# Performance work log

Hardware: AMD Instinct MI355X
Metric: run time of the kernel (lower is better)

## Reference

```python
import jax, jax.numpy as jnp
import numpy as np

H = 256
V = 64
B = 2048
T = 512


def setup_inputs() -> dict:
    key = jax.random.key(0)
    k1, k2, k3 = jax.random.split(key, 3)
    sequential_features = jax.random.normal(k1, (B, T, V), dtype=jnp.float32)
    # kaiming-uniform-like init scale for theta [H, H+V] and theta_dot [1, H]
    bound_t = float(np.sqrt(6.0 / (H + V)))
    theta = jax.random.uniform(k2, (H, H + V), minval=-bound_t, maxval=bound_t, dtype=jnp.float32)
    bound_d = float(np.sqrt(6.0 / H))
    theta_dot = jax.random.uniform(k3, (1, H), minval=-bound_d, maxval=bound_d, dtype=jnp.float32)
    bias = jnp.zeros((1,), dtype=jnp.float32)
    return {"sequential_features": sequential_features, "theta": theta, "bias": bias, "theta_dot": theta_dot}


def reference(sequential_features, theta, bias, theta_dot):
    # sequential_features: [B, T, V]; theta: [H, H+V]; bias: [1]; theta_dot: [1, H]
    Bn = sequential_features.shape[0]
    Hn = theta.shape[0]

    def step(state, token):
        # state: [B, H], token: [B, V]
        st = jnp.concatenate([state, token], axis=1)          # [B, H+V]
        z = st @ theta.T + bias                                # [B, H]
        mean = jnp.mean(z, axis=1, keepdims=True)
        std = jnp.std(z, axis=1, keepdims=True, ddof=1)        # torch.std uses Bessel correction
        z = (z - mean) / std
        return jax.nn.relu(z), None

    xs = jnp.swapaxes(sequential_features, 0, 1)               # [T, B, V]
    init = jnp.zeros((Bn, Hn), dtype=sequential_features.dtype)
    state, _ = jax.lax.scan(step, init, xs)
    logits = jnp.sum(state * theta_dot, axis=1)                # [B]
    return jax.nn.sigmoid(logits)
```

## Files before the change

kernel.cpp:

```cpp
#include <hip/hip_runtime.h>


#define TT 512
#define VV 64
#define HH 256
#define STRD 264

typedef short bf16x8 __attribute__((ext_vector_type(8)));
typedef float f32x4  __attribute__((ext_vector_type(4)));

__device__ __forceinline__ unsigned short f2bf(float f) {
    unsigned int u = __float_as_uint(f);
    return (unsigned short)((u + 0x8000u) >> 16);
}

__device__ __forceinline__ float bf2f(unsigned short u) {
    return __uint_as_float(((unsigned int)u) << 16);
}

__device__ __forceinline__ bf16x8 pack8(float4 a, float4 b) {
    bf16x8 v;
    v[0] = (short)f2bf(a.x); v[1] = (short)f2bf(a.y);
    v[2] = (short)f2bf(a.z); v[3] = (short)f2bf(a.w);
    v[4] = (short)f2bf(b.x); v[5] = (short)f2bf(b.y);
    v[6] = (short)f2bf(b.z); v[7] = (short)f2bf(b.w);
    return v;
}

template <int CTRL>
__device__ __forceinline__ float dppadd(float x) {
    int y = __builtin_amdgcn_update_dpp(0, __float_as_int(x), CTRL, 0xF, 0xF, false);
    return x + __int_as_float(y);
}

template <int CTRL>
__device__ __forceinline__ float dppbcast(float x) {
    int y = __builtin_amdgcn_update_dpp(0, __float_as_int(x), CTRL, 0xF, 0xF, true);
    return __int_as_float(y);
}

__device__ __forceinline__ void barrier_lgkm() {
    asm volatile("s_waitcnt lgkmcnt(0)\n\ts_barrier" ::: "memory");
}

extern "C" __global__ void __launch_bounds__(256, 1)
rnn_scan_kernel(const float* __restrict__ seq,
                const float* __restrict__ theta,
                const float* __restrict__ theta_dot,
                float* __restrict__ out)
{
    __shared__ unsigned short stbuf[2][16][STRD];
    __shared__ __align__(16) float2 partials[64];

    const int tid = threadIdx.x;
    const int w   = tid >> 6;
    const int l   = tid & 63;
    const int q   = l >> 4;
    const int loc = l & 15;
    const int r0  = blockIdx.x << 4;

    bf16x8 bfrag[10][4];
#pragma unroll
    for (int s = 0; s < 4; ++s) {
        const float* trow = theta + (size_t)(w * 64 + s * 16 + loc) * 320;
#pragma unroll
        for (int ks = 0; ks < 10; ++ks) {
            float4 f0 = *(const float4*)(trow + ks * 32 + q * 8);
            float4 f1 = *(const float4*)(trow + ks * 32 + q * 8 + 4);
            bfrag[ks][s] = pack8(f0, f1);
        }
    }

    {
        const int m = tid >> 4, c = (tid & 15) * 16;
        uint4 z = make_uint4(0u, 0u, 0u, 0u);
        *(uint4*)(&stbuf[0][m][c])     = z;
        *(uint4*)(&stbuf[0][m][c + 8]) = z;
    }

    const float* srow = seq + (size_t)(r0 + loc) * (TT * VV);
    float4 tk0 = *(const float4*)(srow + q * 8);
    float4 tk1 = *(const float4*)(srow + q * 8 + 4);
    float4 tk2 = *(const float4*)(srow + 32 + q * 8);
    float4 tk3 = *(const float4*)(srow + 32 + q * 8 + 4);

    __syncthreads();

#pragma unroll 1
    for (int t = 0; t < TT; ++t) {
        unsigned short* stc = &stbuf[t & 1][0][0];
        unsigned short* stn = &stbuf[(t + 1) & 1][0][0];

        bf16x8 a8 = pack8(tk0, tk1);
        bf16x8 a9 = pack8(tk2, tk3);

        if (t + 1 < TT) {
            const float* p = srow + (size_t)(t + 1) * VV;
            tk0 = *(const float4*)(p + q * 8);
            tk1 = *(const float4*)(p + q * 8 + 4);
            tk2 = *(const float4*)(p + 32 + q * 8);
            tk3 = *(const float4*)(p + 32 + q * 8 + 4);
        }

        f32x4 acc[4];
#pragma unroll
        for (int s = 0; s < 4; ++s) { acc[s][0] = 0.f; acc[s][1] = 0.f; acc[s][2] = 0.f; acc[s][3] = 0.f; }

        const unsigned short* arow = stc + loc * STRD;
#pragma unroll
        for (int ks = 0; ks < 8; ++ks) {
            bf16x8 av = *(const bf16x8*)(arow + ks * 32 + q * 8);
#pragma unroll
            for (int s = 0; s < 4; ++s)
                acc[s] = __builtin_amdgcn_mfma_f32_16x16x32_bf16(av, bfrag[ks][s], acc[s], 0, 0, 0);
        }
#pragma unroll
        for (int s = 0; s < 4; ++s)
            acc[s] = __builtin_amdgcn_mfma_f32_16x16x32_bf16(a8, bfrag[8][s], acc[s], 0, 0, 0);
#pragma unroll
        for (int s = 0; s < 4; ++s)
            acc[s] = __builtin_amdgcn_mfma_f32_16x16x32_bf16(a9, bfrag[9][s], acc[s], 0, 0, 0);

        float sum[4], ssq[4];
#pragma unroll
        for (int r = 0; r < 4; ++r) {
            sum[r] = acc[0][r] + acc[1][r] + acc[2][r] + acc[3][r];
            ssq[r] = acc[0][r] * acc[0][r] + acc[1][r] * acc[1][r]
                   + acc[2][r] * acc[2][r] + acc[3][r] * acc[3][r];
        }
#pragma unroll
        for (int r = 0; r < 4; ++r) {
            sum[r] = dppadd<0xB1>(sum[r]);  ssq[r] = dppadd<0xB1>(ssq[r]);
            sum[r] = dppadd<0x4E>(sum[r]);  ssq[r] = dppadd<0x4E>(ssq[r]);
            sum[r] = dppadd<0x124>(sum[r]); ssq[r] = dppadd<0x124>(ssq[r]);
            sum[r] = dppadd<0x128>(sum[r]); ssq[r] = dppadd<0x128>(ssq[r]);
        }
        if (loc < 4)
            partials[((q * 4 + loc) << 2) | w] = make_float2(sum[loc], ssq[loc]);

        barrier_lgkm();

        const int myrow = (q << 2) | (loc & 3);
        float4 pA = *(const float4*)(&partials[myrow << 2]);
        float4 pB = *(const float4*)(&partials[(myrow << 2) | 2]);
        float sumT = (pA.x + pA.z) + (pB.x + pB.z);
        float ssqT = (pA.y + pA.w) + (pB.y + pB.w);
        float mean = sumT * (1.0f / 256.0f);
        float var  = (ssqT - sumT * mean) * (1.0f / 255.0f);
        float rstd = rsqrtf(var);
        float nb   = -mean * rstd;

        float rs[4], nbv[4];
        rs[0] = dppbcast<0x00>(rstd); nbv[0] = dppbcast<0x00>(nb);
        rs[1] = dppbcast<0x55>(rstd); nbv[1] = dppbcast<0x55>(nb);
        rs[2] = dppbcast<0xAA>(rstd); nbv[2] = dppbcast<0xAA>(nb);
        rs[3] = dppbcast<0xFF>(rstd); nbv[3] = dppbcast<0xFF>(nb);

#pragma unroll
        for (int s = 0; s < 4; ++s) {
#pragma unroll
            for (int r = 0; r < 4; ++r) {
                float v = fmaf(acc[s][r], rs[r], nbv[r]);
                v = fmaxf(v, 0.0f);
                stn[(q * 4 + r) * STRD + (w * 64 + s * 16 + loc)] = f2bf(v);
            }
        }
        barrier_lgkm();
    }

    {
        const int m = tid >> 4, c0 = (tid & 15) << 4;
        const unsigned short* sr = &stbuf[0][m][c0];
        float dot = 0.0f;
#pragma unroll
        for (int j = 0; j < 16; ++j)
            dot += bf2f(sr[j]) * theta_dot[c0 + j];
        dot += __shfl_xor(dot, 1, 64);
        dot += __shfl_xor(dot, 2, 64);
        dot += __shfl_xor(dot, 4, 64);
        dot += __shfl_xor(dot, 8, 64);
        if ((tid & 15) == 0)
            out[r0 + m] = 1.0f / (1.0f + expf(-dot));
    }
}

extern "C" void kernel_launch(void* const* d_in, const int* in_sizes, int n_in,
                              void* d_out, int out_size, void* d_ws, size_t ws_size,
                              hipStream_t stream) {
    const float* seq   = (const float*)d_in[0];
    const float* theta = (const float*)d_in[1];
    const float* tdot  = (const float*)d_in[3];
    float* out = (float*)d_out;

    rnn_scan_kernel<<<dim3(128), dim3(256), 0, stream>>>(seq, theta, tdot, out);
}
```

Baseline: 850.7 us.

## Halve rows per block, defer rstd scaling, and precompute token projection off critical path

Each block now handles 8 batch rows instead of 16 and the grid doubles to 256 blocks, padding the MFMA M-dimension with duplicated rows so more CUs run the serial scan. The normalization is split: the state written each step is only mean-centred and ReLU'd, and the per-row rstd is applied to the next step's recurrent matmul result (and to the final dot product), which takes rsqrt and its broadcast off the store path. The token-projection MFMAs for the next step are issued between the partial-sum barrier and the state store to overlap with the reduction. The risks are wasted MFMA work on the padded rows, a bf16 state stored before scaling with a different dynamic range, and higher register pressure under launch_bounds(256,2).

```diff
diff --git a/kernel.cpp b/kernel.cpp
--- a/kernel.cpp
+++ b/kernel.cpp
@@ -3,7 +3,6 @@
 
 #define TT 512
 #define VV 64
-#define HH 256
 #define STRD 264
 
 typedef short bf16x8 __attribute__((ext_vector_type(8)));
@@ -43,7 +42,7 @@
     asm volatile("s_waitcnt lgkmcnt(0)\n\ts_barrier" ::: "memory");
 }
 
-extern "C" __global__ void __launch_bounds__(256, 1)
+extern "C" __global__ void __launch_bounds__(256, 2)
 rnn_scan_kernel(const float* __restrict__ seq,
                 const float* __restrict__ theta,
                 const float* __restrict__ theta_dot,
@@ -51,13 +50,14 @@
 {
     __shared__ unsigned short stbuf[2][16][STRD];
     __shared__ __align__(16) float2 partials[64];
+    __shared__ float rstd_lds[16];
 
     const int tid = threadIdx.x;
     const int w   = tid >> 6;
     const int l   = tid & 63;
     const int q   = l >> 4;
     const int loc = l & 15;
-    const int r0  = blockIdx.x << 4;
+    const int r0  = blockIdx.x << 3;
 
     bf16x8 bfrag[10][4];
 #pragma unroll
@@ -76,14 +76,38 @@
         uint4 z = make_uint4(0u, 0u, 0u, 0u);
         *(uint4*)(&stbuf[0][m][c])     = z;
         *(uint4*)(&stbuf[0][m][c + 8]) = z;
-    }
-
-    const float* srow = seq + (size_t)(r0 + loc) * (TT * VV);
+        *(uint4*)(&stbuf[1][m][c])     = z;
+        *(uint4*)(&stbuf[1][m][c + 8]) = z;
+    }
+
+    const float* srow = seq + (size_t)(r0 + (loc & 7)) * (TT * VV);
     float4 tk0 = *(const float4*)(srow + q * 8);
     float4 tk1 = *(const float4*)(srow + q * 8 + 4);
     float4 tk2 = *(const float4*)(srow + 32 + q * 8);
     float4 tk3 = *(const float4*)(srow + 32 + q * 8 + 4);
 
+    f32x4 acc_t[4];
+    {
+        bf16x8 a8 = pack8(tk0, tk1);
+        bf16x8 a9 = pack8(tk2, tk3);
+        f32x4 zc; zc[0] = 0.f; zc[1] = 0.f; zc[2] = 0.f; zc[3] = 0.f;
+#pragma unroll
+        for (int s = 0; s < 4; ++s) {
+            acc_t[s] = __builtin_amdgcn_mfma_f32_16x16x32_bf16(a8, bfrag[8][s], zc, 0, 0, 0);
+            acc_t[s] = __builtin_amdgcn_mfma_f32_16x16x32_bf16(a9, bfrag[9][s], acc_t[s], 0, 0, 0);
+        }
+    }
+    {
+        const float* p = srow + VV;
+        tk0 = *(const float4*)(p + q * 8);
+        tk1 = *(const float4*)(p + q * 8 + 4);
+        tk2 = *(const float4*)(p + 32 + q * 8);
+        tk3 = *(const float4*)(p + 32 + q * 8 + 4);
+    }
+
+    float rs[4];
+    rs[0] = 1.0f; rs[1] = 1.0f; rs[2] = 1.0f; rs[3] = 1.0f;
+
     __syncthreads();
 
 #pragma unroll 1
@@ -91,17 +115,6 @@
         unsigned short* stc = &stbuf[t & 1][0][0];
         unsigned short* stn = &stbuf[(t + 1) & 1][0][0];
 
-        bf16x8 a8 = pack8(tk0, tk1);
-        bf16x8 a9 = pack8(tk2, tk3);
-
-        if (t + 1 < TT) {
-            const float* p = srow + (size_t)(t + 1) * VV;
-            tk0 = *(const float4*)(p + q * 8);
-            tk1 = *(const float4*)(p + q * 8 + 4);
-            tk2 = *(const float4*)(p + 32 + q * 8);
-            tk3 = *(const float4*)(p + 32 + q * 8 + 4);
-        }
-
         f32x4 acc[4];
 #pragma unroll
         for (int s = 0; s < 4; ++s) { acc[s][0] = 0.f; acc[s][1] = 0.f; acc[s][2] = 0.f; acc[s][3] = 0.f; }
@@ -114,12 +127,12 @@
             for (int s = 0; s < 4; ++s)
                 acc[s] = __builtin_amdgcn_mfma_f32_16x16x32_bf16(av, bfrag[ks][s], acc[s], 0, 0, 0);
         }
+
 #pragma unroll
         for (int s = 0; s < 4; ++s)
-            acc[s] = __builtin_amdgcn_mfma_f32_16x16x32_bf16(a8, bfrag[8][s], acc[s], 0, 0, 0);
-#pragma unroll
-        for (int s = 0; s < 4; ++s)
-            acc[s] = __builtin_amdgcn_mfma_f32_16x16x32_bf16(a9, bfrag[9][s], acc[s], 0, 0, 0);
+#pragma unroll
+            for (int r = 0; r < 4; ++r)
+                acc[s][r] = fmaf(acc[s][r], rs[r], acc_t[s][r]);
 
         float sum[4], ssq[4];
 #pragma unroll
@@ -143,30 +156,61 @@
         const int myrow = (q << 2) | (loc & 3);
         float4 pA = *(const float4*)(&partials[myrow << 2]);
         float4 pB = *(const float4*)(&partials[(myrow << 2) | 2]);
+
+        if (t + 1 < TT) {
+            bf16x8 a8 = pack8(tk0, tk1);
+            bf16x8 a9 = pack8(tk2, tk3);
+            f32x4 zc; zc[0] = 0.f; zc[1] = 0.f; zc[2] = 0.f; zc[3] = 0.f;
+#pragma unroll
+            for (int s = 0; s < 4; ++s) {
+                acc_t[s] = __builtin_amdgcn_mfma_f32_16x16x32_bf16(a8, bfrag[8][s], zc, 0, 0, 0);
+                acc_t[s] = __builtin_amdgcn_mfma_f32_16x16x32_bf16(a9, bfrag[9][s], acc_t[s], 0, 0, 0);
+            }
+            if (t + 2 < TT) {
+                const float* p = srow + (size_t)(t + 2) * VV;
+                tk0 = *(const float4*)(p + q * 8);
+                tk1 = *(const float4*)(p + q * 8 + 4);
+                tk2 = *(const float4*)(p + 32 + q * 8);
+                tk3 = *(const float4*)(p + 32 + q * 8 + 4);
+            }
+        }
+
         float sumT = (pA.x + pA.z) + (pB.x + pB.z);
         float ssqT = (pA.y + pA.w) + (pB.y + pB.w);
         float mean = sumT * (1.0f / 256.0f);
+        float nm   = -mean;
+        float mb[4];
+        mb[0] = dppbcast<0x00>(nm);
+        mb[1] = dppbcast<0x55>(nm);
+        mb[2] = dppbcast<0xAA>(nm);
+        mb[3] = dppbcast<0xFF>(nm);
+
+        if (q < 2) {
+#pragma unroll
+            for (int s = 0; s < 4; ++s)
+#pragma unroll
+                for (int r = 0; r < 4; ++r) {
+                    float v = fmaxf(acc[s][r] + mb[r], 0.0f);
+                    stn[(q * 4 + r) * STRD + (w * 64 + s * 16 + loc)] = f2bf(v);
+                }
+        }
+
         float var  = (ssqT - sumT * mean) * (1.0f / 255.0f);
         float rstd = rsqrtf(var);
-        float nb   = -mean * rstd;
-
-        float rs[4], nbv[4];
-        rs[0] = dppbcast<0x00>(rstd); nbv[0] = dppbcast<0x00>(nb);
-        rs[1] = dppbcast<0x55>(rstd); nbv[1] = dppbcast<0x55>(nb);
-        rs[2] = dppbcast<0xAA>(rstd); nbv[2] = dppbcast<0xAA>(nb);
-        rs[3] = dppbcast<0xFF>(rstd); nbv[3] = dppbcast<0xFF>(nb);
-
-#pragma unroll
-        for (int s = 0; s < 4; ++s) {
-#pragma unroll
-            for (int r = 0; r < 4; ++r) {
-                float v = fmaf(acc[s][r], rs[r], nbv[r]);
-                v = fmaxf(v, 0.0f);
-                stn[(q * 4 + r) * STRD + (w * 64 + s * 16 + loc)] = f2bf(v);
-            }
-        }
+        rs[0] = dppbcast<0x00>(rstd);
+        rs[1] = dppbcast<0x55>(rstd);
+        rs[2] = dppbcast<0xAA>(rstd);
+        rs[3] = dppbcast<0xFF>(rstd);
+
         barrier_lgkm();
     }
+
+    if (w == 0 && loc == 0) {
+#pragma unroll
+        for (int r = 0; r < 4; ++r)
+            rstd_lds[q * 4 + r] = rs[r];
+    }
+    __syncthreads();
 
     {
         const int m = tid >> 4, c0 = (tid & 15) << 4;
@@ -179,8 +223,8 @@
         dot += __shfl_xor(dot, 2, 64);
         dot += __shfl_xor(dot, 4, 64);
         dot += __shfl_xor(dot, 8, 64);
-        if ((tid & 15) == 0)
-            out[r0 + m] = 1.0f / (1.0f + expf(-dot));
+        if ((tid & 15) == 0 && m < 8)
+            out[r0 + m] = 1.0f / (1.0f + expf(-rstd_lds[m] * dot));
     }
 }
 
@@ -192,5 +236,5 @@
     const float* tdot  = (const float*)d_in[3];
     float* out = (float*)d_out;
 
-    rnn_scan_kernel<<<dim3(128), dim3(256), 0, stream>>>(seq, theta, tdot, out);
-}
+    rnn_scan_kernel<<<dim3(256), dim3(256), 0, stream>>>(seq, theta, tdot, out);
+}
```

After: 880.0 us. 3.4% more time.

## Defer layernorm into next step's A-fragment load, removing one barrier per step

Applied to the files above, without the earlier changes.

Each step now stores the raw pre-normalization MFMA outputs to LDS, packed as bf16 with a permuted hidden-column layout. The next step computes mean and rstd from double-buffered partials and applies normalize plus ReLU while building the A fragments. This halves the block barriers per timestep, and the token MFMAs are issued first so they overlap the LDS reads. It also switches to the hardware v_cvt_pk_bf16_f32 packed conversion. The costs are extra ALU work per fragment, a permuted theta gather at setup, and the raw (un-normalized) state being rounded to bf16 before normalization, which slightly changes precision.

```diff
diff --git a/kernel.cpp b/kernel.cpp
--- a/kernel.cpp
+++ b/kernel.cpp
@@ -3,15 +3,15 @@
 
 #define TT 512
 #define VV 64
-#define HH 256
 #define STRD 264
 
 typedef short bf16x8 __attribute__((ext_vector_type(8)));
 typedef float f32x4  __attribute__((ext_vector_type(4)));
 
-__device__ __forceinline__ unsigned short f2bf(float f) {
-    unsigned int u = __float_as_uint(f);
-    return (unsigned short)((u + 0x8000u) >> 16);
+__device__ __forceinline__ unsigned int cvtpk(float lo, float hi) {
+    unsigned int r;
+    asm("v_cvt_pk_bf16_f32 %0, %1, %2" : "=v"(r) : "v"(lo), "v"(hi));
+    return r;
 }
 
 __device__ __forceinline__ float bf2f(unsigned short u) {
@@ -19,24 +19,29 @@
 }
 
 __device__ __forceinline__ bf16x8 pack8(float4 a, float4 b) {
-    bf16x8 v;
-    v[0] = (short)f2bf(a.x); v[1] = (short)f2bf(a.y);
-    v[2] = (short)f2bf(a.z); v[3] = (short)f2bf(a.w);
-    v[4] = (short)f2bf(b.x); v[5] = (short)f2bf(b.y);
-    v[6] = (short)f2bf(b.z); v[7] = (short)f2bf(b.w);
-    return v;
+    union { unsigned int u[4]; bf16x8 v; } r;
+    r.u[0] = cvtpk(a.x, a.y); r.u[1] = cvtpk(a.z, a.w);
+    r.u[2] = cvtpk(b.x, b.y); r.u[3] = cvtpk(b.z, b.w);
+    return r.v;
+}
+
+__device__ __forceinline__ bf16x8 normfrag(const unsigned int* rw, float a, float b) {
+    union { unsigned int u[4]; bf16x8 v; } r;
+#pragma unroll
+    for (int i = 0; i < 4; ++i) {
+        float lo = __uint_as_float(rw[i] << 16);
+        float hi = __uint_as_float(rw[i] & 0xffff0000u);
+        lo = fmaxf(fmaf(lo, a, b), 0.0f);
+        hi = fmaxf(fmaf(hi, a, b), 0.0f);
+        r.u[i] = cvtpk(lo, hi);
+    }
+    return r.v;
 }
 
 template <int CTRL>
 __device__ __forceinline__ float dppadd(float x) {
     int y = __builtin_amdgcn_update_dpp(0, __float_as_int(x), CTRL, 0xF, 0xF, false);
     return x + __int_as_float(y);
-}
-
-template <int CTRL>
-__device__ __forceinline__ float dppbcast(float x) {
-    int y = __builtin_amdgcn_update_dpp(0, __float_as_int(x), CTRL, 0xF, 0xF, true);
-    return __int_as_float(y);
 }
 
 __device__ __forceinline__ void barrier_lgkm() {
@@ -50,7 +55,7 @@
                 float* __restrict__ out)
 {
     __shared__ unsigned short stbuf[2][16][STRD];
-    __shared__ __align__(16) float2 partials[64];
+    __shared__ __align__(16) float2 partials[2][16][4];
 
     const int tid = threadIdx.x;
     const int w   = tid >> 6;
@@ -64,9 +69,23 @@
     for (int s = 0; s < 4; ++s) {
         const float* trow = theta + (size_t)(w * 64 + s * 16 + loc) * 320;
 #pragma unroll
-        for (int ks = 0; ks < 10; ++ks) {
-            float4 f0 = *(const float4*)(trow + ks * 32 + q * 8);
-            float4 f1 = *(const float4*)(trow + ks * 32 + q * 8 + 4);
+        for (int ks = 0; ks < 8; ++ks) {
+            float v[8];
+#pragma unroll
+            for (int j = 0; j < 8; ++j) {
+                int p = ks * 32 + q * 8 + j;
+                int c = ((p & 15) << 4) | (p >> 4);
+                v[j] = trow[c];
+            }
+            union { unsigned int u[4]; bf16x8 b; } r;
+            r.u[0] = cvtpk(v[0], v[1]); r.u[1] = cvtpk(v[2], v[3]);
+            r.u[2] = cvtpk(v[4], v[5]); r.u[3] = cvtpk(v[6], v[7]);
+            bfrag[ks][s] = r.b;
+        }
+#pragma unroll
+        for (int ks = 8; ks < 10; ++ks) {
+            float4 f0 = *(const float4*)(trow + 256 + (ks - 8) * 32 + q * 8);
+            float4 f1 = *(const float4*)(trow + 256 + (ks - 8) * 32 + q * 8 + 4);
             bfrag[ks][s] = pack8(f0, f1);
         }
     }
@@ -77,6 +96,8 @@
         *(uint4*)(&stbuf[0][m][c])     = z;
         *(uint4*)(&stbuf[0][m][c + 8]) = z;
     }
+    if (tid < 64)
+        partials[0][tid >> 2][tid & 3] = make_float2(0.0f, (tid & 3) == 0 ? 255.0f : 0.0f);
 
     const float* srow = seq + (size_t)(r0 + loc) * (TT * VV);
     float4 tk0 = *(const float4*)(srow + q * 8);
@@ -88,11 +109,24 @@
 
 #pragma unroll 1
     for (int t = 0; t < TT; ++t) {
-        unsigned short* stc = &stbuf[t & 1][0][0];
-        unsigned short* stn = &stbuf[(t + 1) & 1][0][0];
+        const unsigned short* stc = &stbuf[t & 1][0][0];
+        unsigned short*       stn = &stbuf[(t + 1) & 1][0][0];
+        const int pb = t & 1;
+
+        float4 qa = *(const float4*)(&partials[pb][loc][0]);
+        float4 qb = *(const float4*)(&partials[pb][loc][2]);
 
         bf16x8 a8 = pack8(tk0, tk1);
         bf16x8 a9 = pack8(tk2, tk3);
+        f32x4 acc[4];
+        {
+            f32x4 zc; zc[0] = 0.f; zc[1] = 0.f; zc[2] = 0.f; zc[3] = 0.f;
+#pragma unroll
+            for (int s = 0; s < 4; ++s) {
+                acc[s] = __builtin_amdgcn_mfma_f32_16x16x32_bf16(a8, bfrag[8][s], zc, 0, 0, 0);
+                acc[s] = __builtin_amdgcn_mfma_f32_16x16x32_bf16(a9, bfrag[9][s], acc[s], 0, 0, 0);
+            }
+        }
 
         if (t + 1 < TT) {
             const float* p = srow + (size_t)(t + 1) * VV;
@@ -102,24 +136,26 @@
             tk3 = *(const float4*)(p + 32 + q * 8 + 4);
         }
 
-        f32x4 acc[4];
-#pragma unroll
-        for (int s = 0; s < 4; ++s) { acc[s][0] = 0.f; acc[s][1] = 0.f; acc[s][2] = 0.f; acc[s][3] = 0.f; }
-
+        uint4 rawf[8];
         const unsigned short* arow = stc + loc * STRD;
 #pragma unroll
+        for (int ks = 0; ks < 8; ++ks)
+            rawf[ks] = *(const uint4*)(arow + ks * 32 + q * 8);
+
+        float sumT = (qa.x + qa.z) + (qb.x + qb.z);
+        float ssqT = (qa.y + qa.w) + (qb.y + qb.w);
+        float mean = sumT * (1.0f / 256.0f);
+        float var  = (ssqT - sumT * mean) * (1.0f / 255.0f);
+        float a_   = rsqrtf(var);
+        float b_   = -mean * a_;
+
+#pragma unroll
         for (int ks = 0; ks < 8; ++ks) {
-            bf16x8 av = *(const bf16x8*)(arow + ks * 32 + q * 8);
+            bf16x8 av = normfrag((const unsigned int*)&rawf[ks], a_, b_);
 #pragma unroll
             for (int s = 0; s < 4; ++s)
                 acc[s] = __builtin_amdgcn_mfma_f32_16x16x32_bf16(av, bfrag[ks][s], acc[s], 0, 0, 0);
         }
-#pragma unroll
-        for (int s = 0; s < 4; ++s)
-            acc[s] = __builtin_amdgcn_mfma_f32_16x16x32_bf16(a8, bfrag[8][s], acc[s], 0, 0, 0);
-#pragma unroll
-        for (int s = 0; s < 4; ++s)
-            acc[s] = __builtin_amdgcn_mfma_f32_16x16x32_bf16(a9, bfrag[9][s], acc[s], 0, 0, 0);
 
         float sum[4], ssq[4];
 #pragma unroll
@@ -136,50 +172,45 @@
             sum[r] = dppadd<0x128>(sum[r]); ssq[r] = dppadd<0x128>(ssq[r]);
         }
         if (loc < 4)
-            partials[((q * 4 + loc) << 2) | w] = make_float2(sum[loc], ssq[loc]);
+            partials[pb ^ 1][(q << 2) | loc][w] = make_float2(sum[loc], ssq[loc]);
+
+        {
+            unsigned short* wb = stn + (q * 4) * STRD + loc * 16 + w * 4;
+#pragma unroll
+            for (int r = 0; r < 4; ++r) {
+                uint2 pk;
+                pk.x = cvtpk(acc[0][r], acc[1][r]);
+                pk.y = cvtpk(acc[2][r], acc[3][r]);
+                *(uint2*)(wb + r * STRD) = pk;
+            }
+        }
 
         barrier_lgkm();
-
-        const int myrow = (q << 2) | (loc & 3);
-        float4 pA = *(const float4*)(&partials[myrow << 2]);
-        float4 pB = *(const float4*)(&partials[(myrow << 2) | 2]);
-        float sumT = (pA.x + pA.z) + (pB.x + pB.z);
-        float ssqT = (pA.y + pA.w) + (pB.y + pB.w);
+    }
+
+    {
+        const int m = tid >> 4, j16 = tid & 15;
+        float4 qa = *(const float4*)(&partials[0][m][0]);
+        float4 qb = *(const float4*)(&partials[0][m][2]);
+        float sumT = (qa.x + qa.z) + (qb.x + qb.z);
+        float ssqT = (qa.y + qa.w) + (qb.y + qb.w);
         float mean = sumT * (1.0f / 256.0f);
         float var  = (ssqT - sumT * mean) * (1.0f / 255.0f);
-        float rstd = rsqrtf(var);
-        float nb   = -mean * rstd;
-
-        float rs[4], nbv[4];
-        rs[0] = dppbcast<0x00>(rstd); nbv[0] = dppbcast<0x00>(nb);
-        rs[1] = dppbcast<0x55>(rstd); nbv[1] = dppbcast<0x55>(nb);
-        rs[2] = dppbcast<0xAA>(rstd); nbv[2] = dppbcast<0xAA>(nb);
-        rs[3] = dppbcast<0xFF>(rstd); nbv[3] = dppbcast<0xFF>(nb);
-
-#pragma unroll
-        for (int s = 0; s < 4; ++s) {
-#pragma unroll
-            for (int r = 0; r < 4; ++r) {
-                float v = fmaf(acc[s][r], rs[r], nbv[r]);
-                v = fmaxf(v, 0.0f);
-                stn[(q * 4 + r) * STRD + (w * 64 + s * 16 + loc)] = f2bf(v);
-            }
-        }
-        barrier_lgkm();
-    }
-
-    {
-        const int m = tid >> 4, c0 = (tid & 15) << 4;
-        const unsigned short* sr = &stbuf[0][m][c0];
+        float a_   = rsqrtf(var);
+        float b_   = -mean * a_;
+
+        const unsigned short* sr = &stbuf[0][m][j16 * 16];
         float dot = 0.0f;
 #pragma unroll
-        for (int j = 0; j < 16; ++j)
-            dot += bf2f(sr[j]) * theta_dot[c0 + j];
+        for (int j = 0; j < 16; ++j) {
+            float v = fmaxf(fmaf(bf2f(sr[j]), a_, b_), 0.0f);
+            dot += v * theta_dot[j * 16 + j16];
+        }
         dot += __shfl_xor(dot, 1, 64);
         dot += __shfl_xor(dot, 2, 64);
         dot += __shfl_xor(dot, 4, 64);
         dot += __shfl_xor(dot, 8, 64);
-        if ((tid & 15) == 0)
+        if (j16 == 0)
             out[r0 + m] = 1.0f / (1.0f + expf(-dot));
     }
 }
```

Result: slower. 933.9 us (+9.8%).
